# Kernel tuning notes

Measured on AMD Instinct MI355X. Metric: run time of the kernel, lower is better.

The kernel has to match this reference:

```python
import jax, jax.numpy as jnp
import numpy as np

LN_EPS = 1e-5
L1_EPS = 1e-12  # F.normalize clamp_min eps


def _layernorm(h, g, b):
    mu = h.mean(-1, keepdims=True)
    var = ((h - mu) ** 2).mean(-1, keepdims=True)
    return (h - mu) * jax.lax.rsqrt(var + LN_EPS) * g + b


def _graph(x, wq_w, wq_b, wk_w, wk_b, gcn_w, ln_g, ln_b):
    # x: [..., n, d]
    qx = x @ wq_w.T + wq_b
    kx = x @ wk_w.T + wk_b
    dot = jnp.einsum('...nd,...md->...nm', qx, kx)
    sq = dot * dot
    adj = sq / jnp.maximum(sq.sum(-1, keepdims=True), L1_EPS)  # L1-normalized rows
    for i in range(gcn_w.shape[0]):
        h = adj @ (x @ gcn_w[i])
        x = jax.nn.relu(_layernorm(h, ln_g[i], ln_b[i]))
    return x.mean(-2)  # mean over nodes -> [..., d]


def setup_inputs() -> dict:
    key = jax.random.key(0)
    ks = jax.random.split(key, 12)
    N, FR, B, NF = 16, 32, 50, 768
    L, NC = 2, 400
    s = 1.0 / np.sqrt(NF)
    inp = {
        'feats': jax.random.normal(ks[0], (N, FR, B, NF), jnp.float32),
        'feat_global_single': jax.random.normal(ks[1], (N, NF), jnp.float32),
        'feat_single_previous': jax.random.normal(ks[2], (N, NF), jnp.float32),
        'wq_w': jax.random.normal(ks[3], (NF, NF), jnp.float32) * s,
        'wq_b': jnp.zeros((NF,), jnp.float32),
        'wk_w': jax.random.normal(ks[4], (NF, NF), jnp.float32) * s,
        'wk_b': jnp.zeros((NF,), jnp.float32),
        'gcn_w': jax.random.normal(ks[5], (L, NF, NF), jnp.float32) * s,
        'ln_g': jnp.ones((L, NF), jnp.float32),
        'ln_b': jnp.zeros((L, NF), jnp.float32),
        'fc1_w': jax.random.normal(ks[6], (NF, 2 * NF), jnp.float32) / np.sqrt(2 * NF),
        'fc1_b': jnp.zeros((NF,), jnp.float32),
        'fc2_w': jax.random.normal(ks[7], (NC, NF), jnp.float32) * s,
        'fc2_b': jnp.zeros((NC,), jnp.float32),
        't_c': 0,
    }
    return inp


def reference(feats, feat_global_single, feat_single_previous,
              wq_w, wq_b, wk_w, wk_b, gcn_w, ln_g, ln_b,
              fc1_w, fc1_b, fc2_w, fc2_b, t_c):
    N, FR, B, NF = feats.shape
    x = feats.reshape(N * FR, B, NF)
    # object-level graph (shared weights)
    x = _graph(x, wq_w, wq_b, wk_w, wk_b, gcn_w, ln_g, ln_b)  # [N*FR, NF]
    x = x.reshape(N, FR, NF)
    # frame-level graph (same shared weights)
    x = _graph(x, wq_w, wq_b, wk_w, wk_b, gcn_w, ln_g, ln_b)  # [N, NF]
    y = jnp.concatenate([x, feat_global_single], axis=-1)      # [N, 2*NF]
    # ClassifierSimple (dropout = identity in eval)
    h = jax.nn.relu(y @ fc1_w.T + fc1_b)
    logits = h @ fc2_w.T + fc2_b
    return (logits, y)
```

## Files before the change

### kernel.cpp

```cpp
#include <hip/hip_runtime.h>
#include <hip/hip_bf16.h>

typedef unsigned short u16;
typedef unsigned int   u32;
typedef __attribute__((ext_vector_type(8))) short short8;
typedef __attribute__((ext_vector_type(4))) float float4v;

__device__ __forceinline__ float bf2f(u16 u){ union{u32 i; float f;} c; c.i = ((u32)u) << 16; return c.f; }
__device__ __forceinline__ float bflo(u32 u){ union{u32 i; float f;} c; c.i = u << 16; return c.f; }
__device__ __forceinline__ float bfhi(u32 u){ union{u32 i; float f;} c; c.i = u & 0xFFFF0000u; return c.f; }
__device__ __forceinline__ u16 f2bf(float f){
  union{float f; u32 i;} c; c.f = f; u32 x = c.i;
  return (u16)((x + 0x7FFFu + ((x >> 16) & 1u)) >> 16);
}
__device__ __forceinline__ u32 pack2(float a, float b){
  union { __hip_bfloat162 h; u32 u; } c;
  c.h = __float22bfloat162_rn(float2{a, b});
  return c.u;
}

__device__ __forceinline__ void async16(const void* g, void* l){
  __builtin_amdgcn_global_load_lds((const __attribute__((address_space(1))) void*)g,
                                   (__attribute__((address_space(3))) void*)l, 16, 0, 0);
}

__global__ void __launch_bounds__(256) conv_bf16(const float* __restrict__ src, u16* __restrict__ dst, int n8)
{
  int t = blockIdx.x * 256 + threadIdx.x;
  int stride = gridDim.x * 256;
  for (int i = t; i < n8; i += stride) {
    float4 a = ((const float4*)src)[2 * i];
    float4 b = ((const float4*)src)[2 * i + 1];
    uint4 o = { pack2(a.x, a.y), pack2(a.z, a.w), pack2(b.x, b.y), pack2(b.z, b.w) };
    ((uint4*)dst)[i] = o;
  }
}

__global__ void transpose_bf16(const float* __restrict__ src, u16* __restrict__ dst)
{
  __shared__ float tile[32][33];
  int r0 = blockIdx.y * 32, c0 = blockIdx.x * 32;
  int tx = threadIdx.x, ty = threadIdx.y;
  for (int i = 0; i < 32; i += 8) tile[ty + i][tx] = src[(size_t)(r0 + ty + i) * 768 + c0 + tx];
  __syncthreads();
  for (int i = 0; i < 32; i += 8) dst[(size_t)(c0 + ty + i) * 768 + r0 + tx] = f2bf(tile[tx][ty + i]);
}

__global__ void prep_gcnT(const float* __restrict__ gcn, u16* __restrict__ QHB, u16* __restrict__ gcnT1)
{
  __shared__ float tile[32][33];
  int l = blockIdx.z;
  int d0 = blockIdx.y * 32, o0 = blockIdx.x * 32;
  int tx = threadIdx.x, ty = threadIdx.y;
  const float* src = gcn + (size_t)l * 589824;
  u16* dst = (l == 0) ? (QHB + (size_t)768 * 768) : gcnT1;
  for (int i = 0; i < 32; i += 8) tile[ty + i][tx] = src[(size_t)(d0 + ty + i) * 768 + o0 + tx];
  __syncthreads();
  for (int i = 0; i < 32; i += 8) dst[(size_t)(o0 + ty + i) * 768 + d0 + tx] = f2bf(tile[tx][ty + i]);
}

__global__ void __launch_bounds__(256) prep_uv(const float* __restrict__ wq, const float* __restrict__ wk,
                                               const float* __restrict__ wqb, const float* __restrict__ wkb,
                                               float* __restrict__ uv, float* __restrict__ cbuf)
{
  if (blockIdx.x < 6) {
    int t = blockIdx.x * 256 + threadIdx.x;
    if (t < 768) {
      float a = 0.f;
      for (int o = 0; o < 768; o++) a += wq[(size_t)o * 768 + t] * wkb[o];
      uv[t] = a;
    } else {
      int d = t - 768;
      float a = 0.f;
      for (int o = 0; o < 768; o++) a += wk[(size_t)o * 768 + d] * wqb[o];
      uv[t] = a;
    }
  } else {
    __shared__ float red[256];
    float a = 0.f;
    for (int o = threadIdx.x; o < 768; o += 256) a += wqb[o] * wkb[o];
    red[threadIdx.x] = a; __syncthreads();
    if (threadIdx.x == 0) { float s = 0.f; for (int i = 0; i < 256; i++) s += red[i]; cbuf[0] = s; }
  }
}

__global__ void __launch_bounds__(256) row_pq(const u16* __restrict__ X, const float* __restrict__ uv,
                                              const float* __restrict__ cbuf, float* __restrict__ p,
                                              float* __restrict__ q, int Mrows)
{
  __shared__ float us[768], vs[768];
  int tid = threadIdx.x, lane = tid & 63, w = tid >> 6;
  for (int i = tid; i < 768; i += 256) { us[i] = uv[i]; vs[i] = uv[768 + i]; }
  __syncthreads();
  int row = blockIdx.x * 4 + w;
  if (row >= Mrows) return;
  const u16* xr = X + (size_t)row * 768;
  float ap = 0.f, aq = 0.f;
  for (int k = 0; k < 12; k++) {
    int d = k * 64 + lane;
    float x = bf2f(xr[d]);
    ap += x * us[d]; aq += x * vs[d];
  }
  for (int m = 1; m <= 32; m <<= 1) { ap += __shfl_xor(ap, m); aq += __shfl_xor(aq, m); }
  if (lane == 0) { p[row] = ap + cbuf[0]; q[row] = aq; }
}

__global__ void __launch_bounds__(256) gemm_bt(const u16* __restrict__ A, const u16* __restrict__ Bw,
                                               const float* __restrict__ bias, u16* __restrict__ C,
                                               int M, int N, int K)
{
  __shared__ __attribute__((aligned(16))) u16 As[128 * 64];
  __shared__ __attribute__((aligned(16))) u16 Bs[128 * 64];
  int tid = threadIdx.x, lane = tid & 63, wid = tid >> 6;
  int wm = wid >> 1, wn = wid & 1;
  size_t m0 = (size_t)blockIdx.x * 128, n0 = (size_t)blockIdx.y * 128;

  float4v acc[4][4];
  for (int r = 0; r < 4; r++) for (int c = 0; c < 4; c++) acc[r][c] = (float4v){0.f, 0.f, 0.f, 0.f};

  int srow8  = lane >> 3;
  int schunk = (lane & 7) ^ srow8;
  const u16* gA[4]; const u16* gB[4];
  u16* lA[4]; u16* lB[4];
#pragma unroll
  for (int j = 0; j < 4; j++) {
    int r = 32 * wid + 8 * j + srow8;
    gA[j] = A  + (m0 + r) * (size_t)K + schunk * 8;
    gB[j] = Bw + (n0 + r) * (size_t)K + schunk * 8;
    lA[j] = &As[(32 * wid + 8 * j) * 64];
    lB[j] = &Bs[(32 * wid + 8 * j) * 64];
  }

  int l15 = lane & 15, quad = lane >> 4;
  int s0 = quad ^ (l15 & 7);

  for (int kt = 0; kt < K; kt += 64) {
#pragma unroll
    for (int j = 0; j < 4; j++) {
      async16(gA[j] + kt, lA[j]);
      async16(gB[j] + kt, lB[j]);
    }
    __syncthreads();
#pragma unroll
    for (int ks = 0; ks < 2; ks++) {
      int so = (s0 ^ (ks << 2)) * 8;
      short8 af[4], bfr[4];
#pragma unroll
      for (int r = 0; r < 4; r++) af[r]  = *(const short8*)&As[(wm * 64 + r * 16 + l15) * 64 + so];
#pragma unroll
      for (int c = 0; c < 4; c++) bfr[c] = *(const short8*)&Bs[(wn * 64 + c * 16 + l15) * 64 + so];
#pragma unroll
      for (int r = 0; r < 4; r++)
#pragma unroll
        for (int c = 0; c < 4; c++)
          acc[r][c] = __builtin_amdgcn_mfma_f32_16x16x32_bf16(af[r], bfr[c], acc[r][c], 0, 0, 0);
    }
    __syncthreads();
  }

  int quad4 = quad * 4;
  for (int c = 0; c < 4; c++) {
    int n = (int)n0 + wn * 64 + c * 16 + l15;
    float bv = bias ? bias[n] : 0.f;
    for (int r = 0; r < 4; r++) {
      size_t mbase = m0 + wm * 64 + r * 16 + quad4;
      for (int t = 0; t < 4; t++)
        C[(mbase + t) * (size_t)N + n] = f2bf(acc[r][c][t] + bv);
    }
  }
}


template<int NP>
__global__ void __launch_bounds__(512) fused_l1(const u16* __restrict__ TH, const u16* __restrict__ AR,
                                                const float* __restrict__ pb, const float* __restrict__ qb,
                                                const float* __restrict__ lng, const float* __restrict__ lnb,
                                                u16* __restrict__ adjG, u16* __restrict__ X, int n)
{
  constexpr int ST = 72;
  constexpr int TPW = (NP == 64) ? 2 : 1;
  __shared__ __attribute__((aligned(16))) u16 adjb[NP * ST];
  __shared__ __attribute__((aligned(16))) u16 HT[2][64 * ST];
  __shared__ float rsum[NP];
  __shared__ float stats[NP][2];
  __shared__ float bc[NP][2];
  __shared__ float ps[NP], qs[NP];
  __shared__ float lg[768], lb[768];

  int g = blockIdx.x;
  int tid = threadIdx.x, lane = tid & 63, w = tid >> 6;
  int l15 = lane & 15, quad = lane >> 4;

  for (int i = tid; i < 768; i += 512) { lg[i] = lng[i]; lb[i] = lnb[i]; }
  if (tid < NP) {
    rsum[tid] = 0.f; stats[tid][0] = 0.f; stats[tid][1] = 0.f;
    ps[tid] = (tid < n) ? pb[(size_t)g * n + tid] : 0.f;
    qs[tid] = (tid < n) ? qb[(size_t)g * n + tid] : 0.f;
  }
  __syncthreads();

  int mt, nt0; bool s_act;
  if (NP == 64) { mt = w & 3; nt0 = (w >> 2) * 2; s_act = true; }
  else          { mt = w & 1; nt0 = w >> 1;       s_act = (w < 4); }

  int rowA = mt * 16 + l15;
  bool aok = rowA < n;
  const u16* tA  = TH + ((size_t)g * n + rowA) * 1536 + quad * 8;
  int rowB0 = (nt0) * 16 + l15, rowB1 = (nt0 + TPW - 1) * 16 + l15;
  bool b0ok = rowB0 < n, b1ok = rowB1 < n;
  const u16* pB0 = AR + ((size_t)g * n + rowB0) * 768 + quad * 8;
  const u16* pB1 = AR + ((size_t)g * n + rowB1) * 768 + quad * 8;

  float4v sacc[TPW];
  for (int j = 0; j < TPW; j++) sacc[j] = (float4v){0.f, 0.f, 0.f, 0.f};

  if (s_act) {
    for (int kt = 0; kt < 768; kt += 32) {
      uint4 av = {0,0,0,0}, bv0 = {0,0,0,0}, bv1 = {0,0,0,0};
      if (aok)  av  = *(const uint4*)(tA + kt);
      if (b0ok) bv0 = *(const uint4*)(pB0 + kt);
      if (TPW == 2 && b1ok) bv1 = *(const uint4*)(pB1 + kt);
      short8 a = *(short8*)&av;
      sacc[0] = __builtin_amdgcn_mfma_f32_16x16x32_bf16(a, *(short8*)&bv0, sacc[0], 0, 0, 0);
      if (TPW == 2)
        sacc[1] = __builtin_amdgcn_mfma_f32_16x16x32_bf16(a, *(short8*)&bv1, sacc[1], 0, 0, 0);
    }
    for (int j = 0; j < TPW; j++) {
      int col = (nt0 + j) * 16 + l15;
      bool cok = col < n;
      for (int t = 0; t < 4; t++) {
        int row = mt * 16 + quad * 4 + t;
        sacc[j][t] = cok ? (sacc[j][t] + ps[row] + qs[col]) : 0.f;
      }
    }
    for (int t = 0; t < 4; t++) {
      float s = 0.f;
      for (int j = 0; j < TPW; j++) { float v = sacc[j][t]; s += v * v; }
      s += __shfl_xor(s, 1); s += __shfl_xor(s, 2); s += __shfl_xor(s, 4); s += __shfl_xor(s, 8);
      if (l15 == 0) atomicAdd(&rsum[mt * 16 + quad * 4 + t], s);
    }
  }
  __syncthreads();
  if (tid < NP) rsum[tid] = 1.0f / fmaxf(rsum[tid], 1e-12f);
  __syncthreads();
  if (s_act) {
    u16* gadj = adjG + (size_t)g * NP * NP;
    for (int j = 0; j < TPW; j++)
      for (int t = 0; t < 4; t++) {
        int row = mt * 16 + quad * 4 + t, col = (nt0 + j) * 16 + l15;
        float v = sacc[j][t];
        u16 b = f2bf(v * v * rsum[row]);
        adjb[row * ST + col] = b;
        gadj[row * NP + col] = b;
      }
  }
  __syncthreads();

  int m2, nt20;
  if (NP == 64) { m2 = w & 3; nt20 = (w >> 2) * 2; }
  else          { m2 = w & 1; nt20 = w >> 1; }

  float4v xacc[12][TPW];
#pragma unroll
  for (int ch = 0; ch < 12; ch++) for (int j = 0; j < TPW; j++) xacc[ch][j] = (float4v){0.f,0.f,0.f,0.f};

  int hj  = tid & (NP - 1);
  int hseg= (NP == 64) ? w : ((tid >> 5) & 7);
  bool hact = (NP == 64) ? true : (tid < NP * 8);
  const u16* hbase = TH + ((size_t)g * n + hj) * 1536 + 768 + hseg * 8;

  uint4 hcur = {0,0,0,0};
  if (hact && hj < n) hcur = *(const uint4*)(hbase);

#pragma unroll
  for (int ch = 0; ch < 12; ch++) {
    uint4 hnext = {0,0,0,0};
    if (ch < 11 && hact && hj < n) hnext = *(const uint4*)(hbase + (ch + 1) * 64);
    u16* htb = HT[ch & 1];
    if (hact) {
      const u16* ep = (const u16*)&hcur;
      for (int i = 0; i < 8; i++) htb[(hseg * 8 + i) * ST + hj] = ep[i];
    }
    __syncthreads();
    for (int k = 0; k < NP / 32; k++) {
      short8 a = *(const short8*)&adjb[(m2 * 16 + l15) * ST + k * 32 + quad * 8];
      for (int j = 0; j < TPW; j++) {
        short8 b = *(const short8*)&htb[((nt20 + j) * 16 + l15) * ST + k * 32 + quad * 8];
        xacc[ch][j] = __builtin_amdgcn_mfma_f32_16x16x32_bf16(a, b, xacc[ch][j], 0, 0, 0);
      }
    }
    hcur = hnext;
  }

  float ssum[4] = {0,0,0,0}, ssq[4] = {0,0,0,0};
#pragma unroll
  for (int ch = 0; ch < 12; ch++)
    for (int j = 0; j < TPW; j++)
      for (int t = 0; t < 4; t++) { float v = xacc[ch][j][t]; ssum[t] += v; ssq[t] += v * v; }
  for (int m = 1; m <= 8; m <<= 1)
    for (int t = 0; t < 4; t++) { ssum[t] += __shfl_xor(ssum[t], m); ssq[t] += __shfl_xor(ssq[t], m); }
  if (l15 == 0)
    for (int t = 0; t < 4; t++) {
      atomicAdd(&stats[m2 * 16 + quad * 4 + t][0], ssum[t]);
      atomicAdd(&stats[m2 * 16 + quad * 4 + t][1], ssq[t]);
    }
  __syncthreads();
  if (tid < NP) {
    float mu = stats[tid][0] * (1.f / 768.f);
    float var = stats[tid][1] * (1.f / 768.f) - mu * mu;
    bc[tid][0] = mu; bc[tid][1] = rsqrtf(fmaxf(var, 0.f) + 1e-5f);
  }
  __syncthreads();

#pragma unroll
  for (int ch = 0; ch < 12; ch++)
    for (int j = 0; j < TPW; j++)
      for (int t = 0; t < 4; t++) {
        int row = m2 * 16 + quad * 4 + t;
        if (row < n) {
          int d = ch * 64 + (nt20 + j) * 16 + l15;
          float v = fmaxf((xacc[ch][j][t] - bc[row][0]) * bc[row][1] * lg[d] + lb[d], 0.f);
          X[((size_t)g * n + row) * 768 + d] = f2bf(v);
        }
      }
}

template<int NP>
__global__ void __launch_bounds__(512) fused_l2(const u16* __restrict__ adjG, const u16* __restrict__ H,
                                                const float* __restrict__ lng, const float* __restrict__ lnb,
                                                u16* __restrict__ Xmean, int n, float inv)
{
  constexpr int ST = 72;
  constexpr int TPW = (NP == 64) ? 2 : 1;
  __shared__ __attribute__((aligned(16))) u16 adjb[NP * ST];
  __shared__ __attribute__((aligned(16))) u16 HT[2][64 * ST];
  __shared__ float stats[NP][2];
  __shared__ float bc[NP][2];
  __shared__ float colsum[768];
  __shared__ float lg[768], lb[768];

  int g = blockIdx.x;
  int tid = threadIdx.x, lane = tid & 63, w = tid >> 6;
  int l15 = lane & 15, quad = lane >> 4;

  for (int i = tid; i < 768; i += 512) { lg[i] = lng[i]; lb[i] = lnb[i]; colsum[i] = 0.f; }
  if (tid < NP) { stats[tid][0] = 0.f; stats[tid][1] = 0.f; }
  if (tid * 8 < NP * NP) {
    int row = (tid * 8) / NP, c0 = (tid * 8) % NP;
    uint4 v = *(const uint4*)(adjG + (size_t)g * NP * NP + row * NP + c0);
    *(uint4*)&adjb[row * ST + c0] = v;
  }

  int m2, nt20;
  if (NP == 64) { m2 = w & 3; nt20 = (w >> 2) * 2; }
  else          { m2 = w & 1; nt20 = w >> 1; }

  float4v xacc[12][TPW];
#pragma unroll
  for (int ch = 0; ch < 12; ch++) for (int j = 0; j < TPW; j++) xacc[ch][j] = (float4v){0.f,0.f,0.f,0.f};

  int hj  = tid & (NP - 1);
  int hseg= (NP == 64) ? w : ((tid >> 5) & 7);
  bool hact = (NP == 64) ? true : (tid < NP * 8);
  const u16* hbase = H + ((size_t)g * n + hj) * 768 + hseg * 8;

  uint4 hcur = {0,0,0,0};
  if (hact && hj < n) hcur = *(const uint4*)(hbase);

  __syncthreads();

#pragma unroll
  for (int ch = 0; ch < 12; ch++) {
    uint4 hnext = {0,0,0,0};
    if (ch < 11 && hact && hj < n) hnext = *(const uint4*)(hbase + (ch + 1) * 64);
    u16* htb = HT[ch & 1];
    if (hact) {
      const u16* ep = (const u16*)&hcur;
      for (int i = 0; i < 8; i++) htb[(hseg * 8 + i) * ST + hj] = ep[i];
    }
    __syncthreads();
    for (int k = 0; k < NP / 32; k++) {
      short8 a = *(const short8*)&adjb[(m2 * 16 + l15) * ST + k * 32 + quad * 8];
      for (int j = 0; j < TPW; j++) {
        short8 b = *(const short8*)&htb[((nt20 + j) * 16 + l15) * ST + k * 32 + quad * 8];
        xacc[ch][j] = __builtin_amdgcn_mfma_f32_16x16x32_bf16(a, b, xacc[ch][j], 0, 0, 0);
      }
    }
    hcur = hnext;
  }

  float ssum[4] = {0,0,0,0}, ssq[4] = {0,0,0,0};
#pragma unroll
  for (int ch = 0; ch < 12; ch++)
    for (int j = 0; j < TPW; j++)
      for (int t = 0; t < 4; t++) { float v = xacc[ch][j][t]; ssum[t] += v; ssq[t] += v * v; }
  for (int m = 1; m <= 8; m <<= 1)
    for (int t = 0; t < 4; t++) { ssum[t] += __shfl_xor(ssum[t], m); ssq[t] += __shfl_xor(ssq[t], m); }
  if (l15 == 0)
    for (int t = 0; t < 4; t++) {
      atomicAdd(&stats[m2 * 16 + quad * 4 + t][0], ssum[t]);
      atomicAdd(&stats[m2 * 16 + quad * 4 + t][1], ssq[t]);
    }
  __syncthreads();
  if (tid < NP) {
    float mu = stats[tid][0] * (1.f / 768.f);
    float var = stats[tid][1] * (1.f / 768.f) - mu * mu;
    bc[tid][0] = mu; bc[tid][1] = rsqrtf(fmaxf(var, 0.f) + 1e-5f);
  }
  __syncthreads();

#pragma unroll
  for (int ch = 0; ch < 12; ch++)
    for (int j = 0; j < TPW; j++)
      for (int t = 0; t < 4; t++) {
        int row = m2 * 16 + quad * 4 + t;
        int d = ch * 64 + (nt20 + j) * 16 + l15;
        float v = fmaxf((xacc[ch][j][t] - bc[row][0]) * bc[row][1] * lg[d] + lb[d], 0.f);
        float vm = (row < n) ? v : 0.f;
        vm += __shfl_xor(vm, 16);
        vm += __shfl_xor(vm, 32);
        if (quad == 0) atomicAdd(&colsum[d], vm);
      }
  __syncthreads();
  if (tid < 384)
    ((u32*)Xmean)[(size_t)g * 384 + tid] = pack2(colsum[tid * 2] * inv, colsum[tid * 2 + 1] * inv);
}

__global__ void __launch_bounds__(384) concat_y(const u16* __restrict__ Xm,
                                                const float* __restrict__ fgs, float* __restrict__ yout)
{
  int b = blockIdx.x, tid = threadIdx.x;
  u32 u = ((const u32*)Xm)[(size_t)b * 384 + tid];
  int d0 = tid * 2;
  yout[(size_t)b * 1536 + d0]     = bflo(u);
  yout[(size_t)b * 1536 + d0 + 1] = bfhi(u);
  yout[(size_t)b * 1536 + 768 + d0]     = fgs[(size_t)b * 768 + d0];
  yout[(size_t)b * 1536 + 768 + d0 + 1] = fgs[(size_t)b * 768 + d0 + 1];
}

__global__ void __launch_bounds__(256) fc1_relu(const float* __restrict__ yout,
                                                const float* __restrict__ fc1w, const float* __restrict__ fc1b,
                                                float* __restrict__ h)
{
  int o = blockIdx.x * 4 + (threadIdx.x >> 6);
  int lane = threadIdx.x & 63;
  float acc[16];
  for (int b = 0; b < 16; b++) acc[b] = 0.f;
  const float4* wr = (const float4*)(fc1w + (size_t)o * 1536);
  for (int k4 = lane; k4 < 384; k4 += 64) {
    float4 wv = wr[k4];
    for (int b = 0; b < 16; b++) {
      float4 yv = ((const float4*)(yout + (size_t)b * 1536))[k4];
      acc[b] += wv.x * yv.x + wv.y * yv.y + wv.z * yv.z + wv.w * yv.w;
    }
  }
  for (int m = 1; m <= 32; m <<= 1)
    for (int b = 0; b < 16; b++) acc[b] += __shfl_xor(acc[b], m);
  if (lane < 16) h[(size_t)lane * 768 + o] = fmaxf(acc[lane] + fc1b[o], 0.f);
}

__global__ void __launch_bounds__(256) fc2_out(const float* __restrict__ h,
                                               const float* __restrict__ fc2w, const float* __restrict__ fc2b,
                                               float* __restrict__ logits)
{
  int o = blockIdx.x * 4 + (threadIdx.x >> 6);
  int lane = threadIdx.x & 63;
  float acc[16];
  for (int b = 0; b < 16; b++) acc[b] = 0.f;
  const float4* wr = (const float4*)(fc2w + (size_t)o * 768);
  for (int k4 = lane; k4 < 192; k4 += 64) {
    float4 wv = wr[k4];
    for (int b = 0; b < 16; b++) {
      float4 hv = ((const float4*)(h + (size_t)b * 768))[k4];
      acc[b] += wv.x * hv.x + wv.y * hv.y + wv.z * hv.z + wv.w * hv.w;
    }
  }
  for (int m = 1; m <= 32; m <<= 1)
    for (int b = 0; b < 16; b++) acc[b] += __shfl_xor(acc[b], m);
  if (lane < 16) logits[(size_t)lane * 400 + o] = acc[lane] + fc2b[o];
}

extern "C" void kernel_launch(void* const* d_in, const int* in_sizes, int n_in,
                              void* d_out, int out_size, void* d_ws, size_t ws_size,
                              hipStream_t stream) {
  const float* feats = (const float*)d_in[0];
  const float* fgs   = (const float*)d_in[1];
  const float* wq_w  = (const float*)d_in[3];
  const float* wq_b  = (const float*)d_in[4];
  const float* wk_w  = (const float*)d_in[5];
  const float* wk_b  = (const float*)d_in[6];
  const float* gcn_w = (const float*)d_in[7];
  const float* ln_g  = (const float*)d_in[8];
  const float* ln_b  = (const float*)d_in[9];
  const float* fc1_w = (const float*)d_in[10];
  const float* fc1_b = (const float*)d_in[11];
  const float* fc2_w = (const float*)d_in[12];
  const float* fc2_b = (const float*)d_in[13];
  float* out  = (float*)d_out;
  float* yout = out + 16 * 400;

  char* ws = (char*)d_ws;
  size_t off = 0;
  auto alloc = [&](size_t b){ size_t r = off; off = (off + b + 255) & ~(size_t)255; return r; };
  u16*  QHB    = (u16*) (ws + alloc((size_t)1536 * 768 * 2));
  u16*  gcnT1  = (u16*) (ws + alloc((size_t)768 * 768 * 2));
  u16*  WqT    = (u16*) (ws + alloc((size_t)768 * 768 * 2));
  u16*  WkT    = (u16*) (ws + alloc((size_t)768 * 768 * 2));
  float* uv    = (float*)(ws + alloc((size_t)1536 * 4));
  float* cbuf  = (float*)(ws + alloc((size_t)4));
  u16*  Abf    = (u16*) (ws + alloc((size_t)25600 * 768 * 2));
  float* pObj  = (float*)(ws + alloc((size_t)25600 * 4));
  float* qObj  = (float*)(ws + alloc((size_t)25600 * 4));
  float* pF    = (float*)(ws + alloc((size_t)512 * 4));
  float* qF    = (float*)(ws + alloc((size_t)512 * 4));
  u16*  Xf     = (u16*) (ws + alloc((size_t)512 * 768 * 2));
  u16*  QHf    = (u16*) (ws + alloc((size_t)512 * 1536 * 2));
  u16*  X1f    = (u16*) (ws + alloc((size_t)512 * 768 * 2));
  u16*  H2f    = (u16*) (ws + alloc((size_t)512 * 768 * 2));
  u16*  adjFb  = (u16*) (ws + alloc((size_t)16 * 32 * 32 * 2));
  u16*  Xm     = (u16*) (ws + alloc((size_t)16 * 768 * 2));
  float* hbuf  = (float*)(ws + alloc((size_t)16 * 768 * 4));
  size_t base = off;

  auto need = [&](int GC){
    size_t R = (size_t)GC * 50;
    return base + R * 1536 * 2 + 512 + R * 768 * 2 + 512 + (size_t)GC * 64 * 64 * 2 + 512;
  };
  int GC = 64;
  if (need(512) <= ws_size) GC = 512;
  else if (need(256) <= ws_size) GC = 256;
  else if (need(128) <= ws_size) GC = 128;
  int R = GC * 50;
  size_t off2 = base;
  auto alloc2 = [&](size_t b){ size_t r = off2; off2 = (off2 + b + 255) & ~(size_t)255; return r; };
  u16* QHc   = (u16*)(ws + alloc2((size_t)R * 1536 * 2));
  u16* X1c   = (u16*)(ws + alloc2((size_t)R * 768 * 2));
  u16* adjGc = (u16*)(ws + alloc2((size_t)GC * 64 * 64 * 2));
  u16* H2c   = QHc;

  transpose_bf16<<<dim3(24, 24), dim3(32, 8), 0, stream>>>(wq_w, WqT);
  transpose_bf16<<<dim3(24, 24), dim3(32, 8), 0, stream>>>(wk_w, WkT);
  prep_uv<<<7, 256, 0, stream>>>(wq_w, wk_w, wq_b, wk_b, uv, cbuf);
  gemm_bt<<<dim3(6, 6), 256, 0, stream>>>(WkT, WqT, nullptr, QHB, 768, 768, 768);
  prep_gcnT<<<dim3(24, 24, 2), dim3(32, 8), 0, stream>>>(gcn_w, QHB, gcnT1);
  conv_bf16<<<2048, 256, 0, stream>>>(feats, Abf, 25600 * 768 / 8);
  row_pq<<<6400, 256, 0, stream>>>(Abf, uv, cbuf, pObj, qObj, 25600);

  int nchunks = 512 / GC;
  for (int c = 0; c < nchunks; c++) {
    const u16* fc = Abf + (size_t)c * GC * 50 * 768;
    gemm_bt<<<dim3(R / 128, 12), 256, 0, stream>>>(fc, QHB, nullptr, QHc, R, 1536, 768);
    fused_l1<64><<<GC, 512, 0, stream>>>(QHc, fc, pObj + (size_t)c * GC * 50, qObj + (size_t)c * GC * 50,
                                         ln_g, ln_b, adjGc, X1c, 50);
    gemm_bt<<<dim3(R / 128, 6), 256, 0, stream>>>(X1c, gcnT1, nullptr, H2c, R, 768, 768);
    fused_l2<64><<<GC, 512, 0, stream>>>(adjGc, H2c, ln_g + 768, ln_b + 768,
                                         Xf + (size_t)c * GC * 768, 50, 1.f / 50.f);
  }

  row_pq<<<128, 256, 0, stream>>>(Xf, uv, cbuf, pF, qF, 512);
  gemm_bt<<<dim3(4, 12), 256, 0, stream>>>(Xf, QHB, nullptr, QHf, 512, 1536, 768);
  fused_l1<32><<<16, 512, 0, stream>>>(QHf, Xf, pF, qF, ln_g, ln_b, adjFb, X1f, 32);
  gemm_bt<<<dim3(4, 6), 256, 0, stream>>>(X1f, gcnT1, nullptr, H2f, 512, 768, 768);
  fused_l2<32><<<16, 512, 0, stream>>>(adjFb, H2f, ln_g + 768, ln_b + 768, Xm, 32, 1.f / 32.f);

  concat_y<<<16, 384, 0, stream>>>(Xm, fgs, yout);
  fc1_relu<<<192, 256, 0, stream>>>(yout, fc1_w, fc1_b, hbuf);
  fc2_out<<<100, 256, 0, stream>>>(hbuf, fc2_w, fc2_b, out);
}
```

Measured before the change: 553.0 us.

## Fuse feature conversion with row bias dots and fold prep kernels

```diff
diff --git a/kernel.cpp b/kernel.cpp
--- a/kernel.cpp
+++ b/kernel.cpp
@@ -24,21 +24,15 @@
                                    (__attribute__((address_space(3))) void*)l, 16, 0, 0);
 }
 
-__global__ void __launch_bounds__(256) conv_bf16(const float* __restrict__ src, u16* __restrict__ dst, int n8)
-{
-  int t = blockIdx.x * 256 + threadIdx.x;
-  int stride = gridDim.x * 256;
-  for (int i = t; i < n8; i += stride) {
-    float4 a = ((const float4*)src)[2 * i];
-    float4 b = ((const float4*)src)[2 * i + 1];
-    uint4 o = { pack2(a.x, a.y), pack2(a.z, a.w), pack2(b.x, b.y), pack2(b.z, b.w) };
-    ((uint4*)dst)[i] = o;
-  }
-}
-
-__global__ void transpose_bf16(const float* __restrict__ src, u16* __restrict__ dst)
+__global__ void prep_w(const float* __restrict__ wq, const float* __restrict__ wk,
+                       const float* __restrict__ gcn,
+                       u16* __restrict__ WqT, u16* __restrict__ WkT,
+                       u16* __restrict__ QHB768, u16* __restrict__ gcnT1)
 {
   __shared__ float tile[32][33];
+  int z = blockIdx.z;
+  const float* src = (z == 0) ? wq : (z == 1) ? wk : gcn + (size_t)(z - 2) * 589824;
+  u16* dst = (z == 0) ? WqT : (z == 1) ? WkT : (z == 2) ? QHB768 : gcnT1;
   int r0 = blockIdx.y * 32, c0 = blockIdx.x * 32;
   int tx = threadIdx.x, ty = threadIdx.y;
   for (int i = 0; i < 32; i += 8) tile[ty + i][tx] = src[(size_t)(r0 + ty + i) * 768 + c0 + tx];
@@ -46,63 +40,62 @@
   for (int i = 0; i < 32; i += 8) dst[(size_t)(c0 + ty + i) * 768 + r0 + tx] = f2bf(tile[tx][ty + i]);
 }
 
-__global__ void prep_gcnT(const float* __restrict__ gcn, u16* __restrict__ QHB, u16* __restrict__ gcnT1)
-{
-  __shared__ float tile[32][33];
-  int l = blockIdx.z;
-  int d0 = blockIdx.y * 32, o0 = blockIdx.x * 32;
-  int tx = threadIdx.x, ty = threadIdx.y;
-  const float* src = gcn + (size_t)l * 589824;
-  u16* dst = (l == 0) ? (QHB + (size_t)768 * 768) : gcnT1;
-  for (int i = 0; i < 32; i += 8) tile[ty + i][tx] = src[(size_t)(d0 + ty + i) * 768 + o0 + tx];
-  __syncthreads();
-  for (int i = 0; i < 32; i += 8) dst[(size_t)(o0 + ty + i) * 768 + d0 + tx] = f2bf(tile[tx][ty + i]);
-}
-
-__global__ void __launch_bounds__(256) prep_uv(const float* __restrict__ wq, const float* __restrict__ wk,
-                                               const float* __restrict__ wqb, const float* __restrict__ wkb,
-                                               float* __restrict__ uv, float* __restrict__ cbuf)
-{
-  if (blockIdx.x < 6) {
-    int t = blockIdx.x * 256 + threadIdx.x;
-    if (t < 768) {
-      float a = 0.f;
-      for (int o = 0; o < 768; o++) a += wq[(size_t)o * 768 + t] * wkb[o];
-      uv[t] = a;
-    } else {
-      int d = t - 768;
-      float a = 0.f;
-      for (int o = 0; o < 768; o++) a += wk[(size_t)o * 768 + d] * wqb[o];
-      uv[t] = a;
-    }
+__global__ void __launch_bounds__(256) prep_uv2(const float* __restrict__ wq, const float* __restrict__ wk,
+                                                const float* __restrict__ wqb, const float* __restrict__ wkb,
+                                                float* __restrict__ uv, float* __restrict__ cbuf)
+{
+  __shared__ float red[4][64];
+  __shared__ float r2[256];
+  int b = blockIdx.x, tid = threadIdx.x;
+  if (b < 24) {
+    const float* w  = (b < 12) ? wq : wk;
+    const float* bs = (b < 12) ? wkb : wqb;
+    int out = (b % 12) * 64 + (tid & 63);
+    int oq = tid >> 6;
+    float a = 0.f;
+    for (int o = oq * 192; o < oq * 192 + 192; o++) a += w[(size_t)o * 768 + out] * bs[o];
+    red[oq][tid & 63] = a;
+    __syncthreads();
+    if (tid < 64)
+      uv[((b < 12) ? 0 : 768) + (b % 12) * 64 + tid] = red[0][tid] + red[1][tid] + red[2][tid] + red[3][tid];
   } else {
-    __shared__ float red[256];
     float a = 0.f;
-    for (int o = threadIdx.x; o < 768; o += 256) a += wqb[o] * wkb[o];
-    red[threadIdx.x] = a; __syncthreads();
-    if (threadIdx.x == 0) { float s = 0.f; for (int i = 0; i < 256; i++) s += red[i]; cbuf[0] = s; }
-  }
-}
-
-__global__ void __launch_bounds__(256) row_pq(const u16* __restrict__ X, const float* __restrict__ uv,
-                                              const float* __restrict__ cbuf, float* __restrict__ p,
-                                              float* __restrict__ q, int Mrows)
+    for (int o = tid; o < 768; o += 256) a += wqb[o] * wkb[o];
+    r2[tid] = a; __syncthreads();
+    if (tid == 0) { float s = 0.f; for (int i = 0; i < 256; i++) s += r2[i]; cbuf[0] = s; }
+  }
+}
+
+__global__ void __launch_bounds__(256) conv_pq(const float* __restrict__ src, u16* __restrict__ dst,
+                                               const float* __restrict__ uv, const float* __restrict__ cbuf,
+                                               float* __restrict__ p, float* __restrict__ q)
 {
   __shared__ float us[768], vs[768];
-  int tid = threadIdx.x, lane = tid & 63, w = tid >> 6;
+  int tid = threadIdx.x, lane = tid & 63;
   for (int i = tid; i < 768; i += 256) { us[i] = uv[i]; vs[i] = uv[768 + i]; }
   __syncthreads();
-  int row = blockIdx.x * 4 + w;
-  if (row >= Mrows) return;
-  const u16* xr = X + (size_t)row * 768;
+  size_t rbase = (size_t)blockIdx.x * 8;
+  int row = tid >> 5;
+  int c3  = (tid & 31) * 3;
+  const float* s = src + (rbase + row) * 768 + (size_t)c3 * 8;
+  u16* d = dst + (rbase + row) * 768 + (size_t)c3 * 8;
   float ap = 0.f, aq = 0.f;
-  for (int k = 0; k < 12; k++) {
-    int d = k * 64 + lane;
-    float x = bf2f(xr[d]);
-    ap += x * us[d]; aq += x * vs[d];
-  }
-  for (int m = 1; m <= 32; m <<= 1) { ap += __shfl_xor(ap, m); aq += __shfl_xor(aq, m); }
-  if (lane == 0) { p[row] = ap + cbuf[0]; q[row] = aq; }
+#pragma unroll
+  for (int j = 0; j < 3; j++) {
+    float4 a = ((const float4*)s)[j * 2];
+    float4 b = ((const float4*)s)[j * 2 + 1];
+    uint4 o = { pack2(a.x, a.y), pack2(a.z, a.w), pack2(b.x, b.y), pack2(b.z, b.w) };
+    ((uint4*)d)[j] = o;
+    const float* uu = &us[(c3 + j) * 8];
+    const float* vv = &vs[(c3 + j) * 8];
+    ap += a.x*uu[0] + a.y*uu[1] + a.z*uu[2] + a.w*uu[3] + b.x*uu[4] + b.y*uu[5] + b.z*uu[6] + b.w*uu[7];
+    aq += a.x*vv[0] + a.y*vv[1] + a.z*vv[2] + a.w*vv[3] + b.x*vv[4] + b.y*vv[5] + b.z*vv[6] + b.w*vv[7];
+  }
+  for (int m = 1; m <= 16; m <<= 1) { ap += __shfl_xor(ap, m); aq += __shfl_xor(aq, m); }
+  if ((lane & 31) == 0) {
+    p[rbase + row] = ap + cbuf[0];
+    q[rbase + row] = aq;
+  }
 }
 
 __global__ void __launch_bounds__(256) gemm_bt(const u16* __restrict__ A, const u16* __restrict__ Bw,
@@ -328,7 +321,9 @@
 template<int NP>
 __global__ void __launch_bounds__(512) fused_l2(const u16* __restrict__ adjG, const u16* __restrict__ H,
                                                 const float* __restrict__ lng, const float* __restrict__ lnb,
-                                                u16* __restrict__ Xmean, int n, float inv)
+                                                u16* __restrict__ Xmean, int n, float inv,
+                                                const float* __restrict__ uvg, const float* __restrict__ cbuf,
+                                                float* __restrict__ pOut, float* __restrict__ qOut)
 {
   constexpr int ST = 72;
   constexpr int TPW = (NP == 64) ? 2 : 1;
@@ -338,6 +333,7 @@
   __shared__ float bc[NP][2];
   __shared__ float colsum[768];
   __shared__ float lg[768], lb[768];
+  __shared__ float pr[8][2];
 
   int g = blockIdx.x;
   int tid = threadIdx.x, lane = tid & 63, w = tid >> 6;
@@ -424,6 +420,23 @@
   __syncthreads();
   if (tid < 384)
     ((u32*)Xmean)[(size_t)g * 384 + tid] = pack2(colsum[tid * 2] * inv, colsum[tid * 2 + 1] * inv);
+
+  if (pOut) {
+    float pp = 0.f, qq = 0.f;
+    if (tid < 384) {
+      float x0 = colsum[tid * 2] * inv, x1 = colsum[tid * 2 + 1] * inv;
+      pp = x0 * uvg[tid * 2] + x1 * uvg[tid * 2 + 1];
+      qq = x0 * uvg[768 + tid * 2] + x1 * uvg[768 + tid * 2 + 1];
+    }
+    for (int m = 1; m <= 32; m <<= 1) { pp += __shfl_xor(pp, m); qq += __shfl_xor(qq, m); }
+    if (lane == 0) { pr[w][0] = pp; pr[w][1] = qq; }
+    __syncthreads();
+    if (tid == 0) {
+      float sp = 0.f, sq = 0.f;
+      for (int i = 0; i < 8; i++) { sp += pr[i][0]; sq += pr[i][1]; }
+      pOut[g] = sp + cbuf[0]; qOut[g] = sq;
+    }
+  }
 }
 
 __global__ void __launch_bounds__(384) concat_y(const u16* __restrict__ Xm,
@@ -538,13 +551,11 @@
   u16* adjGc = (u16*)(ws + alloc2((size_t)GC * 64 * 64 * 2));
   u16* H2c   = QHc;
 
-  transpose_bf16<<<dim3(24, 24), dim3(32, 8), 0, stream>>>(wq_w, WqT);
-  transpose_bf16<<<dim3(24, 24), dim3(32, 8), 0, stream>>>(wk_w, WkT);
-  prep_uv<<<7, 256, 0, stream>>>(wq_w, wk_w, wq_b, wk_b, uv, cbuf);
+  prep_w<<<dim3(24, 24, 4), dim3(32, 8), 0, stream>>>(wq_w, wk_w, gcn_w, WqT, WkT,
+                                                      QHB + (size_t)768 * 768, gcnT1);
+  prep_uv2<<<25, 256, 0, stream>>>(wq_w, wk_w, wq_b, wk_b, uv, cbuf);
   gemm_bt<<<dim3(6, 6), 256, 0, stream>>>(WkT, WqT, nullptr, QHB, 768, 768, 768);
-  prep_gcnT<<<dim3(24, 24, 2), dim3(32, 8), 0, stream>>>(gcn_w, QHB, gcnT1);
-  conv_bf16<<<2048, 256, 0, stream>>>(feats, Abf, 25600 * 768 / 8);
-  row_pq<<<6400, 256, 0, stream>>>(Abf, uv, cbuf, pObj, qObj, 25600);
+  conv_pq<<<3200, 256, 0, stream>>>(feats, Abf, uv, cbuf, pObj, qObj);
 
   int nchunks = 512 / GC;
   for (int c = 0; c < nchunks; c++) {
@@ -554,14 +565,15 @@
                                          ln_g, ln_b, adjGc, X1c, 50);
     gemm_bt<<<dim3(R / 128, 6), 256, 0, stream>>>(X1c, gcnT1, nullptr, H2c, R, 768, 768);
     fused_l2<64><<<GC, 512, 0, stream>>>(adjGc, H2c, ln_g + 768, ln_b + 768,
-                                         Xf + (size_t)c * GC * 768, 50, 1.f / 50.f);
-  }
-
-  row_pq<<<128, 256, 0, stream>>>(Xf, uv, cbuf, pF, qF, 512);
+                                         Xf + (size_t)c * GC * 768, 50, 1.f / 50.f,
+                                         uv, cbuf, pF + (size_t)c * GC, qF + (size_t)c * GC);
+  }
+
   gemm_bt<<<dim3(4, 12), 256, 0, stream>>>(Xf, QHB, nullptr, QHf, 512, 1536, 768);
   fused_l1<32><<<16, 512, 0, stream>>>(QHf, Xf, pF, qF, ln_g, ln_b, adjFb, X1f, 32);
   gemm_bt<<<dim3(4, 6), 256, 0, stream>>>(X1f, gcnT1, nullptr, H2f, 512, 768, 768);
-  fused_l2<32><<<16, 512, 0, stream>>>(adjFb, H2f, ln_g + 768, ln_b + 768, Xm, 32, 1.f / 32.f);
+  fused_l2<32><<<16, 512, 0, stream>>>(adjFb, H2f, ln_g + 768, ln_b + 768, Xm, 32, 1.f / 32.f,
+                                       uv, cbuf, nullptr, nullptr);
 
   concat_y<<<16, 384, 0, stream>>>(Xm, fgs, yout);
   fc1_relu<<<192, 256, 0, stream>>>(yout, fc1_w, fc1_b, hbuf);
```

New measurement: 509.8 us. -7.8%, faster.
